# Performance work log

Hardware: AMD Instinct MI355X
Metric: run time of the kernel (lower is better)

The kernel has to match this reference:

```python
import jax, jax.numpy as jnp
import numpy as np

TAGSET = 32
START = 30
STOP = 31
B = 512
S = 2048


def setup_inputs() -> dict:
    key = jax.random.key(0)
    k1, k2, k3 = jax.random.split(key, 3)
    emissions = jax.random.normal(k1, (B, S, TAGSET), dtype=jnp.float32)
    transitions = jax.random.normal(k2, (TAGSET, TAGSET), dtype=jnp.float32)
    # replicate the torch init: no transition into START, none out of STOP
    transitions = transitions.at[START, :].set(-10000.0).at[:, STOP].set(-10000.0)
    tags = jax.random.randint(k3, (B, S), 0, START)  # valid label tags only
    return {"emissions": emissions, "transitions": transitions, "tags": tags}


def _partition(emissions, transitions):
    # CRF forward algorithm (log partition), vectorized scan over time.
    # alphas: [B, T];  transitions[tag, prev_tag]
    alphas0 = transitions[:, START][None, :] + emissions[:, 0]
    def step(alphas, emit_t):  # emit_t: [B, T]
        # scores[b, tag, prev] = e[b, tag] + trans[tag, prev] + alphas[b, prev]
        scores = emit_t[:, :, None] + transitions[None, :, :] + alphas[:, None, :]
        return jax.nn.logsumexp(scores, axis=2), None
    alphas, _ = jax.lax.scan(step, alphas0, jnp.swapaxes(emissions[:, 1:], 0, 1))
    end_scores = alphas + transitions[STOP][None, :]
    return jax.nn.logsumexp(end_scores, axis=1)  # [B]


def _gold_score(emissions, transitions, tags):
    # vectorized _compute_scores with mask = ones
    e_scores = jnp.take_along_axis(emissions, tags[:, :, None], axis=2)[..., 0].sum(axis=1)
    t_scores = transitions[tags[:, 1:], tags[:, :-1]].sum(axis=1)
    t_scores = t_scores + transitions[tags[:, 0], START] + transitions[STOP, tags[:, -1]]
    return e_scores + t_scores  # [B]


def reference(emissions, transitions, tags):
    # neg_log_likelihood = sum_b (log Z_b - score(gold path)_b)
    return jnp.sum(_partition(emissions, transitions) - _gold_score(emissions, transitions, tags))
```

## Files before the change

### kernel.cpp

```cpp
#include <hip/hip_runtime.h>

#define L2E 1.4426950408889634f
#define LN2 0.6931471805599453f

typedef float f32x16 __attribute__((ext_vector_type(16)));
typedef float f32x2  __attribute__((ext_vector_type(2)));
typedef short bf16x8 __attribute__((ext_vector_type(8)));
typedef unsigned int u32x4 __attribute__((ext_vector_type(4)));

__device__ __forceinline__ float dexp2(float x) { return __builtin_amdgcn_exp2f(x); }
__device__ __forceinline__ float dlog2(float x) { return __builtin_amdgcn_logf(x); }

__device__ __forceinline__ unsigned cvtpk(float a, float b) {
    unsigned r;
    asm("v_cvt_pk_bf16_f32 %0, %1, %2" : "=v"(r) : "v"(a), "v"(b));
    return r;
}

__device__ __forceinline__ unsigned pkrne(float a, float b) {
    unsigned ua = __float_as_uint(a), ub = __float_as_uint(b);
    ua += 0x7FFFu + ((ua >> 16) & 1u);
    ub += 0x7FFFu + ((ub >> 16) & 1u);
    return __builtin_amdgcn_perm(ub, ua, 0x07060302u);
}

__global__ __launch_bounds__(1024, 4) void crf_phase_kernel(
    const float* __restrict__ em,
    const float* __restrict__ tr,
    const int*   __restrict__ tgs,
    float*       __restrict__ ws)
{
    __shared__ float s_tr[1024];
    __shared__ unsigned short s_mat[2 * 16 * 1024];
    __shared__ unsigned s_d8[2 * 16 * 64];
    __shared__ float s_vec[64];
    __shared__ float s_base[2][16];
    __shared__ float s_gold[2][16];

    const int tid = threadIdx.x;
    const int b0  = blockIdx.x * 2;
    const int w   = tid >> 6;
    const int l   = tid & 63;
    const int h   = l >> 5;
    const int q   = l & 31;

    s_tr[tid & 1023] = tr[tid & 1023];
    __syncthreads();

    unsigned ea[8];
#pragma unroll
    for (int j = 0; j < 8; ++j) {
        int k0  = 16 * (j >> 2) + 8 * h + 2 * (j & 3);
        int col = (k0 & ~12) | ((k0 & 4) << 1) | ((k0 & 8) >> 1);
        ea[j] = pkrne(dexp2(s_tr[q * 32 + col] * L2E),
                      dexp2(s_tr[q * 32 + col + 1] * L2E));
    }
    const bf16x8 A0 = __builtin_bit_cast(bf16x8, (u32x4){ea[0], ea[1], ea[2], ea[3]});
    const bf16x8 A1 = __builtin_bit_cast(bf16x8, (u32x4){ea[4], ea[5], ea[6], ea[7]});

    f32x16 zro;
#pragma unroll
    for (int z = 0; z < 16; ++z) zro[z] = 0.f;

    const float* ebA = em + ((size_t)b0 * 2048 + (size_t)w * 128) * 32;
    const float* ebB = ebA + (size_t)2048 * 32;
    const int*   tgA = tgs + (size_t)b0 * 2048;
    const int*   tgB = tgA + 2048;

    f32x16 accA, accB;
    float  scA = 1.f, scB = 1.f;
    int    kpA = 0, kpB = 0, sgA = 0, sgB = 0;
    float  goldA = 0.f, goldB = 0.f;
    float4 r0A, r1A, r0B, r1B;
    int    trA = 0, tlA = 0, trB = 0, tlB = 0;
    int    trAn = 0, tlAn = 0, trBn = 0, tlBn = 0;

#pragma unroll
    for (int r = 0; r < 16; ++r) {
        float iv = ((((r & 3) + 8 * (r >> 2) + 4 * h) == q) ? 1.f : 0.f);
        accA[r] = iv; accB[r] = iv;
    }

    auto eload = [&](const float* eb, int blk) -> float4 {
        int bb2 = blk > 15 ? 15 : blk;
        return *(const float4*)(eb + ((bb2 * 8 + (l >> 3)) * 32 + (l & 7) * 4));
    };
    auto tagload = [&](const int* tgp, int cl, int& treg, int& tlast) {
        int c0 = w * 128 + cl * 64;
        int idx = c0 - 1 + l; if (idx < 0) idx = 0;
        treg  = tgp[idx];
        tlast = tgp[c0 + 63];
    };

    r0A = eload(ebA, 0); r1A = eload(ebA, 1);
    r0B = eload(ebB, 0); r1B = eload(ebB, 1);
    tagload(tgA, 0, trA, tlA);
    tagload(tgB, 0, trB, tlB);

#pragma unroll 1
    for (int blk = 0; blk < 16; ++blk) {
        if ((blk & 7) == 0) {
            int cl = blk >> 3;
            int cg = w * 2 + cl;
            if (cl > 0) { trA = trAn; tlA = tlAn; trB = trBn; tlB = tlBn; }
            {
                int sA = __shfl(trA, (l + 1) & 63, 64);
                int cA = (l == 63) ? tlA : sA;
                int pA = trA;
                int sB = __shfl(trB, (l + 1) & 63, 64);
                int cB = (l == 63) ? tlB : sB;
                int pB = trB;
                if (l == 0 && cg == 0) { pA = 30; pB = 30; }
                goldA += s_tr[cA * 32 + pA];
                goldB += s_tr[cB * 32 + pB];
            }
            if (cl < 1) { tagload(tgA, 1, trAn, tlAn); tagload(tgB, 1, trBn, tlBn); }
        }

        {
            int trel = (blk & 7) * 8 + (l >> 3);
            int c = l & 7;
            int slot = w * 64 + (l >> 3) * 8 + (c & 1) * 4 + (c >> 1);
            {
                int tshf = __shfl(trA, (trel + 1) & 63, 64);
                int tgt  = (trel == 63) ? tlA : tshf;
                if ((tgt >> 2) == c) {
                    int sub = tgt & 3;
                    goldA += sub == 0 ? r0A.x : sub == 1 ? r0A.y : sub == 2 ? r0A.z : r0A.w;
                }
                float4 dv;
                dv.x = dexp2(r0A.x * L2E); dv.y = dexp2(r0A.y * L2E);
                dv.z = dexp2(r0A.z * L2E); dv.w = dexp2(r0A.w * L2E);
                unsigned u = (unsigned)__builtin_amdgcn_cvt_pk_fp8_f32(dv.x, dv.y, 0, false);
                u = (unsigned)__builtin_amdgcn_cvt_pk_fp8_f32(dv.z, dv.w, (int)u, true);
                s_d8[slot] = u;
            }
            {
                int tshf = __shfl(trB, (trel + 1) & 63, 64);
                int tgt  = (trel == 63) ? tlB : tshf;
                if ((tgt >> 2) == c) {
                    int sub = tgt & 3;
                    goldB += sub == 0 ? r0B.x : sub == 1 ? r0B.y : sub == 2 ? r0B.z : r0B.w;
                }
                float4 dv;
                dv.x = dexp2(r0B.x * L2E); dv.y = dexp2(r0B.y * L2E);
                dv.z = dexp2(r0B.z * L2E); dv.w = dexp2(r0B.w * L2E);
                unsigned u = (unsigned)__builtin_amdgcn_cvt_pk_fp8_f32(dv.x, dv.y, 0, false);
                u = (unsigned)__builtin_amdgcn_cvt_pk_fp8_f32(dv.z, dv.w, (int)u, true);
                s_d8[1024 + slot] = u;
            }
        }
        r0A = r1A; r1A = eload(ebA, blk + 2);
        r0B = r1B; r1B = eload(ebB, blk + 2);

        const bool skiplast = (blk == 15) && (w == 15);

#pragma unroll
        for (int s = 0; s < 8; ++s) {
            if (s == 7 && skiplast) continue;
#define DO_STEP(ACC, SC, KP, SG, BANK) do { \
            const u32x4 rv = *(const u32x4*)(s_d8 + (BANK) + w * 64 + s * 8 + h * 4); \
            unsigned bbn[8]; \
            _Pragma("unroll") for (int q2 = 0; q2 < 4; ++q2) { \
                f32x2 dlo = __builtin_amdgcn_cvt_pk_f32_fp8((int)rv[q2], false); \
                f32x2 dhi = __builtin_amdgcn_cvt_pk_f32_fp8((int)rv[q2], true); \
                f32x2 a0; a0.x = ACC[4 * q2 + 0]; a0.y = ACC[4 * q2 + 1]; \
                f32x2 a1; a1.x = ACC[4 * q2 + 2]; a1.y = ACC[4 * q2 + 3]; \
                f32x2 m0 = a0 * dlo; \
                f32x2 m1 = a1 * dhi; \
                if (s == 0 || s == 4) { \
                    f32x2 sc; sc.x = SC; sc.y = SC; \
                    m0 = m0 * sc; m1 = m1 * sc; \
                } \
                bbn[2 * q2]     = cvtpk(m0.x, m0.y); \
                bbn[2 * q2 + 1] = cvtpk(m1.x, m1.y); \
            } \
            if (s == 0 || s == 4) SG += KP; \
            bf16x8 B0 = __builtin_bit_cast(bf16x8, (u32x4){bbn[0], bbn[1], bbn[2], bbn[3]}); \
            bf16x8 B1 = __builtin_bit_cast(bf16x8, (u32x4){bbn[4], bbn[5], bbn[6], bbn[7]}); \
            f32x16 t = __builtin_amdgcn_mfma_f32_32x32x16_bf16(A0, B0, zro, 0, 0, 0); \
            ACC = __builtin_amdgcn_mfma_f32_32x32x16_bf16(A1, B1, t, 0, 0, 0); \
            if (s == 3 || s == 7) { \
                unsigned eb = (__float_as_uint(ACC[0]) >> 23) & 0xFF; \
                unsigned ku = (unsigned)__builtin_amdgcn_readfirstlane((int)eb); \
                KP = (int)ku - 127; \
                SC = __uint_as_float((254u - ku) << 23); \
            } \
} while (0)
            DO_STEP(accA, scA, kpA, sgA, 0);
            DO_STEP(accB, scB, kpB, sgB, 1024);
#undef DO_STEP
        }
    }

#pragma unroll
    for (int p = 0; p < 8; ++p) {
        int rrow = ((2 * p) & 3) + 8 * ((2 * p) >> 2) + 4 * h;
        *(unsigned*)(s_mat + w * 1024 + q * 32 + rrow) = pkrne(accA[2 * p], accA[2 * p + 1]);
        *(unsigned*)(s_mat + 16 * 1024 + w * 1024 + q * 32 + rrow) = pkrne(accB[2 * p], accB[2 * p + 1]);
    }
    if (l == 0) { s_base[0][w] = (float)sgA; s_base[1][w] = (float)sgB; }

#pragma unroll
    for (int m = 1; m < 64; m <<= 1) goldA += __shfl_xor(goldA, m, 64);
#pragma unroll
    for (int m = 1; m < 64; m <<= 1) goldB += __shfl_xor(goldB, m, 64);
    if (l == 0) { s_gold[0][w] = goldA; s_gold[1][w] = goldB; }
    __syncthreads();

    if (tid < 64) {
        int h2 = tid >> 5;
        int i  = tid & 31;
        const unsigned short* mat = s_mat + h2 * 16 * 1024;
        const int* tgp = h2 ? tgB : tgA;
        float x  = dexp2(s_tr[i * 32 + 30] * L2E);
        float xb = 0.f, bs = 0.f;
        for (int c = 0; c < 16; ++c) {
            s_vec[h2 * 32 + i] = x;
            float yv[32];
#pragma unroll
            for (int j = 0; j < 8; ++j)
                *(float4*)&yv[4 * j] = *(const float4*)&s_vec[h2 * 32 + 4 * j];
            float a2 = 0.f;
#pragma unroll
            for (int j = 0; j < 32; ++j) {
                unsigned short uv = mat[c * 1024 + j * 32 + i];
                a2 += __uint_as_float((unsigned)uv << 16) * yv[j];
            }
            unsigned eb2 = (__float_as_uint(a2) >> 23) & 0xFF;
            int ku0 = __shfl((int)eb2, 0, 32);
            x  = a2 * __uint_as_float((unsigned)(254 - ku0) << 23);
            xb += (float)(ku0 - 127);
            bs += s_base[h2][c];
        }
        float elast = em[((size_t)(b0 + h2) * 2048 + 2047) * 32 + i];
        float wv = dexp2((s_tr[31 * 32 + i] + elast) * L2E);
        float sv = x * wv;
#pragma unroll
        for (int m2 = 1; m2 < 32; m2 <<= 1) sv += __shfl_xor(sv, m2, 32);
        float logZ = (xb + bs + dlog2(sv)) * LN2;
        if (i == 0) {
            float g = 0.f;
#pragma unroll
            for (int wv2 = 0; wv2 < 16; ++wv2) g += s_gold[h2][wv2];
            g += s_tr[31 * 32 + tgp[2047]];
            ws[b0 + h2] = logZ - g;
        }
    }
}

__global__ __launch_bounds__(64) void crf_reduce_kernel(
    const float* __restrict__ ws, float* __restrict__ out)
{
    int l = threadIdx.x;
    float s = 0.f;
#pragma unroll
    for (int k = 0; k < 8; ++k) s += ws[l + k * 64];
    s += __shfl_xor(s, 1, 64);
    s += __shfl_xor(s, 2, 64);
    s += __shfl_xor(s, 4, 64);
    s += __shfl_xor(s, 8, 64);
    s += __shfl_xor(s, 16, 64);
    s += __shfl_xor(s, 32, 64);
    if (l == 0) out[0] = s;
}

extern "C" void kernel_launch(void* const* d_in, const int* in_sizes, int n_in,
                              void* d_out, int out_size, void* d_ws, size_t ws_size,
                              hipStream_t stream)
{
    const float* em = (const float*)d_in[0];
    const float* tr = (const float*)d_in[1];
    const int*   tg = (const int*)d_in[2];
    float* ws  = (float*)d_ws;
    float* out = (float*)d_out;

    hipLaunchKernelGGL(crf_phase_kernel, dim3(256), dim3(1024), 0, stream, em, tr, tg, ws);
    hipLaunchKernelGGL(crf_reduce_kernel, dim3(1), dim3(64), 0, stream, ws, out);
}
```

Baseline: 101.4 us.

## Switch to rank-one vector propagation after early matrix-product blocks

Each wave still builds its 32x32 chunk transfer matrix with MFMA products for the first four blocks. It then splits that product into a normalized left vector and a column-sum right vector. For the remaining blocks it propagates only that right vector through the time steps, using fp8-packed emissions, DPP max/sum reductions and LDS broadcasts instead of two MFMAs per step. The final cross-chunk combine becomes a chain of dot products with the stored vectors instead of bf16 32x32 matrix-vector products. This relies on products of positive matrices quickly becoming nearly rank-one, which introduces an approximation error, and it adds per-step LDS round trips and cross-lane reductions.

```diff
diff --git a/kernel.cpp b/kernel.cpp
--- a/kernel.cpp
+++ b/kernel.cpp
@@ -23,6 +23,13 @@
     ub += 0x7FFFu + ((ub >> 16) & 1u);
     return __builtin_amdgcn_perm(ub, ua, 0x07060302u);
 }
+
+#define DPPMAXU(m, ctrl) { \
+    unsigned _t = (unsigned)__builtin_amdgcn_update_dpp(0, (int)(m), ctrl, 0xF, 0xF, true); \
+    if (_t > (m)) (m) = _t; }
+#define DPPADDF(x, ctrl) { \
+    int _t = __builtin_amdgcn_update_dpp(0, __float_as_int(x), ctrl, 0xF, 0xF, true); \
+    (x) += __int_as_float(_t); }
 
 __global__ __launch_bounds__(1024, 4) void crf_phase_kernel(
     const float* __restrict__ em,
@@ -31,9 +38,11 @@
     float*       __restrict__ ws)
 {
     __shared__ float s_tr[1024];
-    __shared__ unsigned short s_mat[2 * 16 * 1024];
-    __shared__ unsigned s_d8[2 * 16 * 64];
-    __shared__ float s_vec[64];
+    __shared__ unsigned s_d8[2][16 * 64];
+    __shared__ __align__(16) unsigned char s_w8[2][16 * 32];
+    __shared__ float s_u[16 * 32];
+    __shared__ float s_v[2][16 * 32];
+    __shared__ float s_uf[2][16 * 32];
     __shared__ float s_base[2][16];
     __shared__ float s_gold[2][16];
 
@@ -47,13 +56,15 @@
     s_tr[tid & 1023] = tr[tid & 1023];
     __syncthreads();
 
+    f32x2 efv[8];
     unsigned ea[8];
 #pragma unroll
     for (int j = 0; j < 8; ++j) {
         int k0  = 16 * (j >> 2) + 8 * h + 2 * (j & 3);
         int col = (k0 & ~12) | ((k0 & 4) << 1) | ((k0 & 8) >> 1);
-        ea[j] = pkrne(dexp2(s_tr[q * 32 + col] * L2E),
-                      dexp2(s_tr[q * 32 + col + 1] * L2E));
+        efv[j].x = dexp2(s_tr[q * 32 + col] * L2E);
+        efv[j].y = dexp2(s_tr[q * 32 + col + 1] * L2E);
+        ea[j] = pkrne(efv[j].x, efv[j].y);
     }
     const bf16x8 A0 = __builtin_bit_cast(bf16x8, (u32x4){ea[0], ea[1], ea[2], ea[3]});
     const bf16x8 A1 = __builtin_bit_cast(bf16x8, (u32x4){ea[4], ea[5], ea[6], ea[7]});
@@ -67,11 +78,16 @@
     const int*   tgA = tgs + (size_t)b0 * 2048;
     const int*   tgB = tgA + 2048;
 
+    const int dhD   = (q >> 3) + 4 * ((q >> 2) & 1);
+    const int dhsh  = (q & 3) << 3;
+    const int wperm = 16 * ((q >> 2) & 1) + 4 * (q >> 3) + (q & 3);
+
     f32x16 accA, accB;
     float  scA = 1.f, scB = 1.f;
     int    kpA = 0, kpB = 0, sgA = 0, sgB = 0;
     float  goldA = 0.f, goldB = 0.f;
-    float4 r0A, r1A, r0B, r1B;
+    float  uA = 0.f, uB = 0.f;
+    float4 r0A, r0B;
     int    trA = 0, tlA = 0, trB = 0, tlB = 0;
     int    trAn = 0, tlAn = 0, trBn = 0, tlBn = 0;
 
@@ -82,8 +98,8 @@
     }
 
     auto eload = [&](const float* eb, int blk) -> float4 {
-        int bb2 = blk > 15 ? 15 : blk;
-        return *(const float4*)(eb + ((bb2 * 8 + (l >> 3)) * 32 + (l & 7) * 4));
+        int k = blk > 15 ? 15 : blk;
+        return *(const float4*)(eb + ((k * 8 + (l >> 3)) * 32 + (l & 7) * 4));
     };
     auto tagload = [&](const int* tgp, int cl, int& treg, int& tlast) {
         int c0 = w * 128 + cl * 64;
@@ -91,9 +107,44 @@
         treg  = tgp[idx];
         tlast = tgp[c0 + 63];
     };
-
-    r0A = eload(ebA, 0); r1A = eload(ebA, 1);
-    r0B = eload(ebB, 0); r1B = eload(ebB, 1);
+    auto handoff = [&](const f32x16& ACC, float& UOWN, int vb) {
+        unsigned bbh[8];
+#pragma unroll
+        for (int j = 0; j < 8; ++j) bbh[j] = pkrne(ACC[2 * j], ACC[2 * j + 1]);
+        bf16x8 Bh0 = __builtin_bit_cast(bf16x8, (u32x4){bbh[0], bbh[1], bbh[2], bbh[3]});
+        bf16x8 Bh1 = __builtin_bit_cast(bf16x8, (u32x4){bbh[4], bbh[5], bbh[6], bbh[7]});
+        const unsigned OB = 0x3F803F80u;
+        const bf16x8 Ao = __builtin_bit_cast(bf16x8, (u32x4){OB, OB, OB, OB});
+        f32x16 t2 = __builtin_amdgcn_mfma_f32_32x32x16_bf16(Ao, Bh0, zro, 0, 0, 0);
+        t2 = __builtin_amdgcn_mfma_f32_32x32x16_bf16(Ao, Bh1, t2, 0, 0, 0);
+        float wq = t2[0];
+        float ssum = wq;
+        DPPADDF(ssum, 0xB1) DPPADDF(ssum, 0x4E)
+        DPPADDF(ssum, 0x141) DPPADDF(ssum, 0x140)
+        ssum += __shfl_xor(ssum, 16, 64);
+        if (l < 32) s_v[vb][w * 32 + q] = wq * __builtin_amdgcn_rcpf(ssum);
+        float ur[16];
+#pragma unroll
+        for (int r = 0; r < 16; ++r) {
+            float t3 = ACC[r];
+            DPPADDF(t3, 0xB1) DPPADDF(t3, 0x4E)
+            DPPADDF(t3, 0x141) DPPADDF(t3, 0x140)
+            t3 += __shfl_xor(t3, 16, 64);
+            ur[r] = t3;
+        }
+        if (q == 0) {
+#pragma unroll
+            for (int p = 0; p < 4; ++p) {
+                float4 vv;
+                vv.x = ur[4 * p + 0]; vv.y = ur[4 * p + 1];
+                vv.z = ur[4 * p + 2]; vv.w = ur[4 * p + 3];
+                *(float4*)(s_u + w * 32 + 8 * p + 4 * h) = vv;
+            }
+        }
+        UOWN = s_u[w * 32 + q];
+    };
+
+    r0A = eload(ebA, 0); r0B = eload(ebB, 0);
     tagload(tgA, 0, trA, tlA);
     tagload(tgB, 0, trB, tlB);
 
@@ -117,88 +168,110 @@
             if (cl < 1) { tagload(tgA, 1, trAn, tlAn); tagload(tgB, 1, trBn, tlBn); }
         }
 
-        {
-            int trel = (blk & 7) * 8 + (l >> 3);
-            int c = l & 7;
-            int slot = w * 64 + (l >> 3) * 8 + (c & 1) * 4 + (c >> 1);
-            {
-                int tshf = __shfl(trA, (trel + 1) & 63, 64);
-                int tgt  = (trel == 63) ? tlA : tshf;
-                if ((tgt >> 2) == c) {
-                    int sub = tgt & 3;
-                    goldA += sub == 0 ? r0A.x : sub == 1 ? r0A.y : sub == 2 ? r0A.z : r0A.w;
-                }
-                float4 dv;
-                dv.x = dexp2(r0A.x * L2E); dv.y = dexp2(r0A.y * L2E);
-                dv.z = dexp2(r0A.z * L2E); dv.w = dexp2(r0A.w * L2E);
-                unsigned u = (unsigned)__builtin_amdgcn_cvt_pk_fp8_f32(dv.x, dv.y, 0, false);
-                u = (unsigned)__builtin_amdgcn_cvt_pk_fp8_f32(dv.z, dv.w, (int)u, true);
-                s_d8[slot] = u;
-            }
-            {
-                int tshf = __shfl(trB, (trel + 1) & 63, 64);
-                int tgt  = (trel == 63) ? tlB : tshf;
-                if ((tgt >> 2) == c) {
-                    int sub = tgt & 3;
-                    goldB += sub == 0 ? r0B.x : sub == 1 ? r0B.y : sub == 2 ? r0B.z : r0B.w;
-                }
-                float4 dv;
-                dv.x = dexp2(r0B.x * L2E); dv.y = dexp2(r0B.y * L2E);
-                dv.z = dexp2(r0B.z * L2E); dv.w = dexp2(r0B.w * L2E);
-                unsigned u = (unsigned)__builtin_amdgcn_cvt_pk_fp8_f32(dv.x, dv.y, 0, false);
-                u = (unsigned)__builtin_amdgcn_cvt_pk_fp8_f32(dv.z, dv.w, (int)u, true);
-                s_d8[1024 + slot] = u;
-            }
-        }
-        r0A = r1A; r1A = eload(ebA, blk + 2);
-        r0B = r1B; r1B = eload(ebB, blk + 2);
-
-        const bool skiplast = (blk == 15) && (w == 15);
-
-#pragma unroll
-        for (int s = 0; s < 8; ++s) {
-            if (s == 7 && skiplast) continue;
-#define DO_STEP(ACC, SC, KP, SG, BANK) do { \
-            const u32x4 rv = *(const u32x4*)(s_d8 + (BANK) + w * 64 + s * 8 + h * 4); \
-            unsigned bbn[8]; \
-            _Pragma("unroll") for (int q2 = 0; q2 < 4; ++q2) { \
-                f32x2 dlo = __builtin_amdgcn_cvt_pk_f32_fp8((int)rv[q2], false); \
-                f32x2 dhi = __builtin_amdgcn_cvt_pk_f32_fp8((int)rv[q2], true); \
-                f32x2 a0; a0.x = ACC[4 * q2 + 0]; a0.y = ACC[4 * q2 + 1]; \
-                f32x2 a1; a1.x = ACC[4 * q2 + 2]; a1.y = ACC[4 * q2 + 3]; \
-                f32x2 m0 = a0 * dlo; \
-                f32x2 m1 = a1 * dhi; \
-                if (s == 0 || s == 4) { \
-                    f32x2 sc; sc.x = SC; sc.y = SC; \
-                    m0 = m0 * sc; m1 = m1 * sc; \
+#define STAGE(BANK, R0, TRX, TLX, GOLD) do { \
+            int trel = (blk & 7) * 8 + (l >> 3); \
+            int tshf = __shfl(TRX, (trel + 1) & 63, 64); \
+            int tgt  = (trel == 63) ? TLX : tshf; \
+            if ((tgt >> 2) == (l & 7)) { \
+                int sub = tgt & 3; \
+                GOLD += sub == 0 ? R0.x : sub == 1 ? R0.y : sub == 2 ? R0.z : R0.w; \
+            } \
+            float4 dv; \
+            dv.x = dexp2(R0.x * L2E); dv.y = dexp2(R0.y * L2E); \
+            dv.z = dexp2(R0.z * L2E); dv.w = dexp2(R0.w * L2E); \
+            unsigned uu = (unsigned)__builtin_amdgcn_cvt_pk_fp8_f32(dv.x, dv.y, 0, false); \
+            uu = (unsigned)__builtin_amdgcn_cvt_pk_fp8_f32(dv.z, dv.w, (int)uu, true); \
+            int c = l & 7; \
+            s_d8[BANK][w * 64 + (l >> 3) * 8 + (c & 1) * 4 + (c >> 1)] = uu; \
+} while (0)
+        STAGE(0, r0A, trA, tlA, goldA);
+        STAGE(1, r0B, trB, tlB, goldB);
+#undef STAGE
+        r0A = eload(ebA, blk + 1);
+        r0B = eload(ebB, blk + 1);
+
+        if (blk < 4) {
+#pragma unroll
+            for (int s = 0; s < 8; ++s) {
+#define MSTEP(BANK, ACC, SCUR, KPEND, SIGMA) do { \
+                const u32x4 rv = *(const u32x4*)(&s_d8[BANK][w * 64 + s * 8 + h * 4]); \
+                unsigned bbn[8]; \
+                _Pragma("unroll") for (int q2 = 0; q2 < 4; ++q2) { \
+                    f32x2 dlo = __builtin_amdgcn_cvt_pk_f32_fp8((int)rv[q2], false); \
+                    f32x2 dhi = __builtin_amdgcn_cvt_pk_f32_fp8((int)rv[q2], true); \
+                    f32x2 a0; a0.x = ACC[4 * q2 + 0]; a0.y = ACC[4 * q2 + 1]; \
+                    f32x2 a1; a1.x = ACC[4 * q2 + 2]; a1.y = ACC[4 * q2 + 3]; \
+                    f32x2 m0 = a0 * dlo; \
+                    f32x2 m1 = a1 * dhi; \
+                    if (s == 0 || s == 4) { \
+                        f32x2 sc; sc.x = SCUR; sc.y = SCUR; \
+                        m0 = m0 * sc; m1 = m1 * sc; \
+                    } \
+                    bbn[2 * q2]     = cvtpk(m0.x, m0.y); \
+                    bbn[2 * q2 + 1] = cvtpk(m1.x, m1.y); \
                 } \
-                bbn[2 * q2]     = cvtpk(m0.x, m0.y); \
-                bbn[2 * q2 + 1] = cvtpk(m1.x, m1.y); \
-            } \
-            if (s == 0 || s == 4) SG += KP; \
-            bf16x8 B0 = __builtin_bit_cast(bf16x8, (u32x4){bbn[0], bbn[1], bbn[2], bbn[3]}); \
-            bf16x8 B1 = __builtin_bit_cast(bf16x8, (u32x4){bbn[4], bbn[5], bbn[6], bbn[7]}); \
-            f32x16 t = __builtin_amdgcn_mfma_f32_32x32x16_bf16(A0, B0, zro, 0, 0, 0); \
-            ACC = __builtin_amdgcn_mfma_f32_32x32x16_bf16(A1, B1, t, 0, 0, 0); \
-            if (s == 3 || s == 7) { \
-                unsigned eb = (__float_as_uint(ACC[0]) >> 23) & 0xFF; \
-                unsigned ku = (unsigned)__builtin_amdgcn_readfirstlane((int)eb); \
-                KP = (int)ku - 127; \
-                SC = __uint_as_float((254u - ku) << 23); \
-            } \
+                if (s == 0 || s == 4) SIGMA += KPEND; \
+                bf16x8 B0 = __builtin_bit_cast(bf16x8, (u32x4){bbn[0], bbn[1], bbn[2], bbn[3]}); \
+                bf16x8 B1 = __builtin_bit_cast(bf16x8, (u32x4){bbn[4], bbn[5], bbn[6], bbn[7]}); \
+                f32x16 t = __builtin_amdgcn_mfma_f32_32x32x16_bf16(A0, B0, zro, 0, 0, 0); \
+                ACC = __builtin_amdgcn_mfma_f32_32x32x16_bf16(A1, B1, t, 0, 0, 0); \
+                if (s == 3 || s == 7) { \
+                    unsigned eb2 = (__float_as_uint(ACC[0]) >> 23) & 0xFF; \
+                    unsigned ku = (unsigned)__builtin_amdgcn_readfirstlane((int)eb2); \
+                    KPEND = (int)ku - 127; \
+                    SCUR = __uint_as_float((254u - ku) << 23); \
+                } \
 } while (0)
-            DO_STEP(accA, scA, kpA, sgA, 0);
-            DO_STEP(accB, scB, kpB, sgB, 1024);
-#undef DO_STEP
+                MSTEP(0, accA, scA, kpA, sgA);
+                MSTEP(1, accB, scB, kpB, sgB);
+#undef MSTEP
+            }
+        } else {
+            if (blk == 4) { handoff(accA, uA, 0); handoff(accB, uB, 1); }
+            unsigned drA[8], drB[8];
+#pragma unroll
+            for (int s = 0; s < 8; ++s) {
+                drA[s] = s_d8[0][w * 64 + s * 8 + dhD];
+                drB[s] = s_d8[1][w * 64 + s * 8 + dhD];
+            }
+#pragma unroll
+            for (int s = 0; s < 8; ++s) {
+                if (s == 7 && blk == 15 && w == 15) continue;
+#define VSTEP(BANK, UOWN, SIGMA, DRS) do { \
+                f32x2 dx = __builtin_amdgcn_cvt_pk_f32_fp8((int)((DRS) >> dhsh), false); \
+                float wv = dx.x * UOWN; \
+                unsigned m = __float_as_uint(wv); \
+                DPPMAXU(m, 0xB1) DPPMAXU(m, 0x4E) \
+                DPPMAXU(m, 0x141) DPPMAXU(m, 0x140) \
+                { \
+                    unsigned o16 = (unsigned)__shfl_xor((int)m, 16, 64); \
+                    if (o16 > m) m = o16; \
+                } \
+                unsigned ku = (m >> 23) & 0xFF; \
+                SIGMA += (int)ku - 127; \
+                float wn = wv * __uint_as_float((254u - ku) << 23); \
+                unsigned w8 = (unsigned)__builtin_amdgcn_cvt_pk_fp8_f32(wn, wn, 0, false); \
+                if (l < 32) s_w8[BANK][w * 32 + wperm] = (unsigned char)w8; \
+                const u32x4 W = *(const u32x4*)(&s_w8[BANK][w * 32 + 16 * h]); \
+                f32x2 part; part.x = 0.f; part.y = 0.f; \
+                _Pragma("unroll") for (int g2 = 0; g2 < 4; ++g2) { \
+                    f32x2 lo = __builtin_amdgcn_cvt_pk_f32_fp8((int)W[g2], false); \
+                    f32x2 hi = __builtin_amdgcn_cvt_pk_f32_fp8((int)W[g2], true); \
+                    part += efv[2 * g2] * lo; \
+                    part += efv[2 * g2 + 1] * hi; \
+                } \
+                float p  = part.x + part.y; \
+                float po = __shfl_xor(p, 32, 64); \
+                UOWN = p + po; \
+} while (0)
+                VSTEP(0, uA, sgA, drA[s]);
+                VSTEP(1, uB, sgB, drB[s]);
+#undef VSTEP
+            }
         }
     }
 
-#pragma unroll
-    for (int p = 0; p < 8; ++p) {
-        int rrow = ((2 * p) & 3) + 8 * ((2 * p) >> 2) + 4 * h;
-        *(unsigned*)(s_mat + w * 1024 + q * 32 + rrow) = pkrne(accA[2 * p], accA[2 * p + 1]);
-        *(unsigned*)(s_mat + 16 * 1024 + w * 1024 + q * 32 + rrow) = pkrne(accB[2 * p], accB[2 * p + 1]);
-    }
+    if (l < 32) { s_uf[0][w * 32 + q] = uA; s_uf[1][w * 32 + q] = uB; }
     if (l == 0) { s_base[0][w] = (float)sgA; s_base[1][w] = (float)sgB; }
 
 #pragma unroll
@@ -211,38 +284,28 @@
     if (tid < 64) {
         int h2 = tid >> 5;
         int i  = tid & 31;
-        const unsigned short* mat = s_mat + h2 * 16 * 1024;
         const int* tgp = h2 ? tgB : tgA;
         float x  = dexp2(s_tr[i * 32 + 30] * L2E);
-        float xb = 0.f, bs = 0.f;
+        float xb = 0.f;
         for (int c = 0; c < 16; ++c) {
-            s_vec[h2 * 32 + i] = x;
-            float yv[32];
-#pragma unroll
-            for (int j = 0; j < 8; ++j)
-                *(float4*)&yv[4 * j] = *(const float4*)&s_vec[h2 * 32 + 4 * j];
-            float a2 = 0.f;
-#pragma unroll
-            for (int j = 0; j < 32; ++j) {
-                unsigned short uv = mat[c * 1024 + j * 32 + i];
-                a2 += __uint_as_float((unsigned)uv << 16) * yv[j];
-            }
-            unsigned eb2 = (__float_as_uint(a2) >> 23) & 0xFF;
-            int ku0 = __shfl((int)eb2, 0, 32);
-            x  = a2 * __uint_as_float((unsigned)(254 - ku0) << 23);
-            xb += (float)(ku0 - 127);
-            bs += s_base[h2][c];
+            float t = s_v[h2][c * 32 + i] * x;
+#pragma unroll
+            for (int m2 = 1; m2 < 32; m2 <<= 1) t += __shfl_xor(t, m2, 32);
+            unsigned kb = (__float_as_uint(t) >> 23) & 0xFF;
+            float tn = t * __uint_as_float((254u - kb) << 23);
+            x = s_uf[h2][c * 32 + i] * tn;
+            xb += s_base[h2][c] + (float)((int)kb - 127);
         }
         float elast = em[((size_t)(b0 + h2) * 2048 + 2047) * 32 + i];
-        float wv = dexp2((s_tr[31 * 32 + i] + elast) * L2E);
-        float sv = x * wv;
+        float wv2 = dexp2((s_tr[31 * 32 + i] + elast) * L2E);
+        float sv = x * wv2;
 #pragma unroll
         for (int m2 = 1; m2 < 32; m2 <<= 1) sv += __shfl_xor(sv, m2, 32);
-        float logZ = (xb + bs + dlog2(sv)) * LN2;
+        float logZ = (xb + dlog2(sv)) * LN2;
         if (i == 0) {
             float g = 0.f;
 #pragma unroll
-            for (int wv2 = 0; wv2 < 16; ++wv2) g += s_gold[h2][wv2];
+            for (int wv3 = 0; wv3 < 16; ++wv3) g += s_gold[h2][wv3];
             g += s_tr[31 * 32 + tgp[2047]];
             ws[b0 + h2] = logZ - g;
         }
```

After: 106.6 us. 5.1% more time.
